# Kernel tuning notes

Hardware: AMD Instinct MI355X
Metric: run time of the kernel (lower is better)

Reference implementation:

```python
import jax, jax.numpy as jnp
import numpy as np

T = 8192   # sequence length (= max_seq_len)
E = 1024   # embedding dim
D = 11     # hard-coded projection dim in source


def setup_inputs() -> dict:
    key = jax.random.key(0)
    ks = jax.random.split(key, 6)
    s_e = 1.0 / np.sqrt(E)
    s_d = 1.0 / np.sqrt(D)
    return {
        "x": jax.random.randint(ks[0], (T,), 0, 32000, dtype=jnp.int64),
        "x_embeddings": jax.random.normal(ks[1], (T, E), dtype=jnp.float32),
        "Wk": jax.random.normal(ks[2], (D, E), dtype=jnp.float32) * s_e,
        "bk": jnp.zeros((D,), dtype=jnp.float32),
        "Wq": jax.random.normal(ks[3], (D, E), dtype=jnp.float32) * s_e,
        "bq": jnp.zeros((D,), dtype=jnp.float32),
        "Wv": jax.random.normal(ks[4], (D, E), dtype=jnp.float32) * s_e,
        "bv": jnp.zeros((D,), dtype=jnp.float32),
        "Wf": jax.random.normal(ks[5], (E, D), dtype=jnp.float32) * s_d,
        "bf": jnp.zeros((E,), dtype=jnp.float32),
    }


def reference(x, x_embeddings, Wk, bk, Wq, bq, Wv, bv, Wf, bf):
    t = x.shape[0]  # static under jit
    k = x_embeddings @ Wk.T + bk            # [T, D]
    q = x_embeddings @ Wq.T + bq            # [T, D]
    v = x_embeddings @ Wv.T + bv            # [T, D]
    att = q @ k.T                           # [T, T]; NOTE: no 1/sqrt(D) scaling in source
    causal = jnp.tril(jnp.ones((t, t), dtype=bool))
    att = jnp.where(causal, att, -jnp.inf)
    att = jax.nn.softmax(att, axis=1)       # dim=1 as in source
    res = att @ v                           # [T, D]
    return res @ Wf.T + bf                  # [T, E]
```

## Files before the change

### kernel.cpp

```cpp
#include <hip/hip_runtime.h>

#define T_SEQ 8192
#define E_DIM 1024
#define QS 36
#define NEC 8
#define ECOLS 128
#define KC 64
#define C2N 32
#define XST 65
#define RB 64
#define JCH 64
#define NSLOT 64
#define RPB 512
#define NIB (T_SEQ / RPB)
#define KVW 24
#define TR 16
#define LOG2E 1.4426950408889634f

__device__ __forceinline__ float2 pkfma(float2 a, float2 b, float2 c) {
    return make_float2(fmaf(a.x, b.x, c.x), fmaf(a.y, b.y, c.y));
}
__device__ __forceinline__ float2 f2(float x, float y) { return make_float2(x, y); }


__global__ __launch_bounds__(256) void prep_wf(const float* __restrict__ Wf,
                                               float* __restrict__ Wfp) {
    int id = blockIdx.x * 256 + threadIdx.x;
    if (id >= E_DIM * 12) return;
    int e = id / 12, d = id % 12;
    Wfp[id] = (d < 11) ? Wf[(size_t)e * 11 + d] : 0.f;
}

__global__ __launch_bounds__(256) void qkv_proj(
    const float* __restrict__ xe,
    const float* __restrict__ Wk, const float* __restrict__ bk,
    const float* __restrict__ Wq, const float* __restrict__ bq,
    const float* __restrict__ Wv, const float* __restrict__ bv,
    float* __restrict__ partQ) {
    const int row0 = blockIdx.x * RB;
    const int ec = blockIdx.y;
    const int lane = threadIdx.x & 63;
    const int wg = __builtin_amdgcn_readfirstlane(threadIdx.x >> 6);

    __shared__ float2 xP[C2N * XST];

    const float* wrow[9]; int col[9]; float bias[9]; bool live[9];
#pragma unroll
    for (int k = 0; k < 9; ++k) {
        int o = wg * 9 + k;
        const float* base; float b = 0.f; int c; bool lv = true;
        if (o < 11)      { base = Wk + (size_t)o * E_DIM;        b = bk[o];      c = o; }
        else if (o < 22) { base = Wq + (size_t)(o - 11) * E_DIM; b = bq[o - 11]; c = o + 1; }
        else if (o < 33) { base = Wv + (size_t)(o - 22) * E_DIM; b = bv[o - 22]; c = o + 2; }
        else             { base = Wk; c = (o == 33) ? 11 : (o == 34) ? 23 : 35; lv = false; }
        wrow[k] = base; col[k] = c; bias[k] = b; live[k] = lv;
    }

    float2 acc[9];
#pragma unroll
    for (int k = 0; k < 9; ++k) acc[k] = f2(0.f, 0.f);

    float4 st[4];
#define STAGE_LOAD(sub)                                                         \
    {                                                                           \
        const int cb = ec * ECOLS + (sub) * KC;                                 \
        _Pragma("unroll")                                                       \
        for (int t = 0; t < 4; ++t) {                                           \
            int idx = threadIdx.x + t * 256;                                    \
            int r = idx >> 4, c4 = idx & 15;                                    \
            st[t] = *(const float4*)(xe + (size_t)(row0 + r) * E_DIM + cb + c4 * 4); \
        }                                                                       \
    }

    STAGE_LOAD(0);
    for (int sub = 0; sub < ECOLS / KC; ++sub) {
        if (sub) __syncthreads();
#pragma unroll
        for (int t = 0; t < 4; ++t) {
            int idx = threadIdx.x + t * 256;
            int r = idx >> 4, c4 = idx & 15;
            float2* d = &xP[(size_t)(c4 * 2) * XST + r];
            d[0]   = f2(st[t].x, st[t].y);
            d[XST] = f2(st[t].z, st[t].w);
        }
        if (sub + 1 < ECOLS / KC) STAGE_LOAD(sub + 1);
        __syncthreads();

        const int cbase = ec * ECOLS + sub * KC;
#pragma unroll 4
        for (int c2 = 0; c2 < C2N; ++c2) {
            float2 xv = xP[c2 * XST + lane];
            const int c = cbase + 2 * c2;
#pragma unroll
            for (int k = 0; k < 9; ++k) {
                const float2 wv = *(const float2*)(wrow[k] + c);
                acc[k] = pkfma(xv, wv, acc[k]);
            }
        }
    }
#undef STAGE_LOAD

    float* dst = partQ + ((size_t)ec * T_SEQ + row0 + lane) * QS;
#pragma unroll
    for (int k = 0; k < 9; ++k) {
        float v = acc[k].x + acc[k].y + (ec == 0 ? bias[k] : 0.f);
        dst[col[k]] = live[k] ? v : 0.f;
    }
}

__global__ __launch_bounds__(256) void reduceQ(const float* __restrict__ partQ,
                                               float* __restrict__ qkvF) {
    const size_t idx = (size_t)blockIdx.x * 256 + threadIdx.x;
    const float4* p = (const float4*)partQ;
    const size_t cs = (size_t)T_SEQ * (QS / 4);
    float4 s = make_float4(0.f, 0.f, 0.f, 0.f);
#pragma unroll
    for (int c = 0; c < NEC; ++c) {
        float4 a = p[idx + (size_t)c * cs];
        s.x += a.x; s.y += a.y; s.z += a.z; s.w += a.w;
    }
    ((float4*)qkvF)[idx] = s;
}

__device__ __forceinline__ void attn_chunk(const float* kv, int j0, int r0,
    const float4& qa0, const float4& qa1, const float4& qa2,
    const float4& qb0, const float4& qb1, const float4& qb2,
    float2& a01, float2& a23, float2& a45, float2& a67, float2& a89, float2& aXL,
    float2& b01, float2& b23, float2& b45, float2& b67, float2& b89, float2& bXL) {
#pragma unroll 2
    for (int jj = 0; jj < JCH; ++jj) {
        const float* kp = kv + jj * KVW;
        const float4 kA = *(const float4*)(kp);
        const float4 kB = *(const float4*)(kp + 4);
        const float4 kC = *(const float4*)(kp + 8);
        const float4 vA = *(const float4*)(kp + 12);
        const float4 vB = *(const float4*)(kp + 16);
        const float4 vC = *(const float4*)(kp + 20);

        float2 sa = pkfma(f2(qa0.x, qa0.y), f2(kA.x, kA.y),
                    pkfma(f2(qa0.z, qa0.w), f2(kA.z, kA.w),
                    pkfma(f2(qa1.x, qa1.y), f2(kB.x, kB.y),
                    pkfma(f2(qa1.z, qa1.w), f2(kB.z, kB.w),
                    pkfma(f2(qa2.x, qa2.y), f2(kC.x, kC.y), f2(0.f, 0.f))))));
        float2 sb = pkfma(f2(qb0.x, qb0.y), f2(kA.x, kA.y),
                    pkfma(f2(qb0.z, qb0.w), f2(kA.z, kA.w),
                    pkfma(f2(qb1.x, qb1.y), f2(kB.x, kB.y),
                    pkfma(f2(qb1.z, qb1.w), f2(kB.z, kB.w),
                    pkfma(f2(qb2.x, qb2.y), f2(kC.x, kC.y), f2(0.f, 0.f))))));
        float pa = exp2f(sa.x + sa.y + qa2.z * kC.z);
        float pb = exp2f(sb.x + sb.y + qb2.z * kC.z);
        const int j = j0 + jj;
        pa = (j <= r0)     ? pa : 0.f;
        pb = (j <= r0 + 1) ? pb : 0.f;
        float2 pa2 = f2(pa, pa), pb2 = f2(pb, pb);
        a01 = pkfma(pa2, f2(vA.x, vA.y), a01);
        a23 = pkfma(pa2, f2(vA.z, vA.w), a23);
        a45 = pkfma(pa2, f2(vB.x, vB.y), a45);
        a67 = pkfma(pa2, f2(vB.z, vB.w), a67);
        a89 = pkfma(pa2, f2(vC.x, vC.y), a89);
        aXL = pkfma(pa2, f2(vC.z, 1.f),  aXL);
        b01 = pkfma(pb2, f2(vA.x, vA.y), b01);
        b23 = pkfma(pb2, f2(vA.z, vA.w), b23);
        b45 = pkfma(pb2, f2(vB.x, vB.y), b45);
        b67 = pkfma(pb2, f2(vB.z, vB.w), b67);
        b89 = pkfma(pb2, f2(vC.x, vC.y), b89);
        bXL = pkfma(pb2, f2(vC.z, 1.f),  bXL);
    }
}

__device__ __forceinline__ void stage_kv(const float* __restrict__ qkvF,
                                         float* kv, int j0) {
    for (int idx = threadIdx.x; idx < JCH * 6; idx += 256) {
        int row = idx / 6, f = idx % 6;
        int srcOff = f * 4 + (f >= 3 ? 12 : 0);
        float4 v = *(const float4*)(qkvF + (size_t)(j0 + row) * QS + srcOff);
        *(float4*)(kv + row * KVW + f * 4) = v;
    }
}

__global__ __launch_bounds__(256, 4) void attn(const float* __restrict__ qkvF,
                                               float* __restrict__ part) {
    const int ib = blockIdx.x, jc = blockIdx.y;
    if (jc > 8 * ib + 7) return;
    const int row0 = ib * RPB;
    const int r0 = row0 + threadIdx.x * 2;

    const float* qp0 = qkvF + (size_t)r0 * QS + 12;
    const float* qp1 = qp0 + QS;
    float4 qa0 = *(const float4*)(qp0), qa1 = *(const float4*)(qp0 + 4), qa2 = *(const float4*)(qp0 + 8);
    float4 qb0 = *(const float4*)(qp1), qb1 = *(const float4*)(qp1 + 4), qb2 = *(const float4*)(qp1 + 8);
    qa0.x *= LOG2E; qa0.y *= LOG2E; qa0.z *= LOG2E; qa0.w *= LOG2E;
    qa1.x *= LOG2E; qa1.y *= LOG2E; qa1.z *= LOG2E; qa1.w *= LOG2E;
    qa2.x *= LOG2E; qa2.y *= LOG2E; qa2.z *= LOG2E;
    qb0.x *= LOG2E; qb0.y *= LOG2E; qb0.z *= LOG2E; qb0.w *= LOG2E;
    qb1.x *= LOG2E; qb1.y *= LOG2E; qb1.z *= LOG2E; qb1.w *= LOG2E;
    qb2.x *= LOG2E; qb2.y *= LOG2E; qb2.z *= LOG2E;

    float2 a01 = f2(0.f, 0.f), a23 = a01, a45 = a01, a67 = a01, a89 = a01, aXL = a01;
    float2 b01 = a01, b23 = a01, b45 = a01, b67 = a01, b89 = a01, bXL = a01;

    __shared__ float kv[JCH * KVW];

    const int j0A = jc * JCH;
    stage_kv(qkvF, kv, j0A);
    __syncthreads();
    attn_chunk(kv, j0A, r0, qa0, qa1, qa2, qb0, qb1, qb2,
               a01, a23, a45, a67, a89, aXL, b01, b23, b45, b67, b89, bXL);

    const int j0B = (jc + NSLOT) * JCH;
    if (j0B <= row0 + RPB - 1) {
        __syncthreads();
        stage_kv(qkvF, kv, j0B);
        __syncthreads();
        attn_chunk(kv, j0B, r0, qa0, qa1, qa2, qb0, qb1, qb2,
                   a01, a23, a45, a67, a89, aXL, b01, b23, b45, b67, b89, bXL);
    }

    float* dst = part + ((size_t)jc * T_SEQ + r0) * 12;
    float4 t;
    t.x = a01.x; t.y = a01.y; t.z = a23.x; t.w = a23.y; *(float4*)(dst + 0)  = t;
    t.x = a45.x; t.y = a45.y; t.z = a67.x; t.w = a67.y; *(float4*)(dst + 4)  = t;
    t.x = a89.x; t.y = a89.y; t.z = aXL.x; t.w = aXL.y; *(float4*)(dst + 8)  = t;
    t.x = b01.x; t.y = b01.y; t.z = b23.x; t.w = b23.y; *(float4*)(dst + 12) = t;
    t.x = b45.x; t.y = b45.y; t.z = b67.x; t.w = b67.y; *(float4*)(dst + 16) = t;
    t.x = b89.x; t.y = b89.y; t.z = bXL.x; t.w = bXL.y; *(float4*)(dst + 20) = t;
}

__global__ __launch_bounds__(256) void pass2(const float* __restrict__ part,
                                             const float* __restrict__ Wfp,
                                             const float* __restrict__ bf,
                                             float* __restrict__ out) {
    const int t0 = blockIdx.x * TR;
    __shared__ float res[TR][12];
    int cnt = t0 / JCH + 1;
    if (cnt > NSLOT) cnt = NSLOT;
    if (threadIdx.x < TR * 12) {
        const float* p = part + (size_t)t0 * 12 + threadIdx.x;
        const size_t S = (size_t)T_SEQ * 12;
        float v[8];
#pragma unroll
        for (int u = 0; u < 8; ++u) v[u] = 0.f;
        int c = 0;
        for (; c + 8 <= cnt; c += 8) {
#pragma unroll
            for (int u = 0; u < 8; ++u) v[u] += p[(size_t)(c + u) * S];
        }
        for (; c < cnt; ++c) v[0] += p[(size_t)c * S];
        float s = ((v[0] + v[1]) + (v[2] + v[3])) + ((v[4] + v[5]) + (v[6] + v[7]));
        const int d = threadIdx.x % 12;
        res[threadIdx.x / 12][d] = (d == 11) ? (1.f / s) : s;
    }
    __syncthreads();

    const int e0 = threadIdx.x * 4;
    float4 wf[4][3];
#pragma unroll
    for (int ee = 0; ee < 4; ++ee) {
        const float4* wp = (const float4*)(Wfp + (size_t)(e0 + ee) * 12);
        wf[ee][0] = wp[0]; wf[ee][1] = wp[1]; wf[ee][2] = wp[2];
    }
    const float4 bv = *(const float4*)(bf + e0);

    for (int r = 0; r < TR; ++r) {
        float rr[12];
#pragma unroll
        for (int d = 0; d < 12; ++d) rr[d] = res[r][d];
        float2 a0 = f2(0.f, 0.f), a1 = a0, a2 = a0, a3 = a0;
#pragma unroll
        for (int d = 0; d < 10; d += 2) {
            float2 rv = f2(rr[d], rr[d + 1]);
            a0 = pkfma(rv, f2(((const float*)&wf[0][0])[d], ((const float*)&wf[0][0])[d + 1]), a0);
            a1 = pkfma(rv, f2(((const float*)&wf[1][0])[d], ((const float*)&wf[1][0])[d + 1]), a1);
            a2 = pkfma(rv, f2(((const float*)&wf[2][0])[d], ((const float*)&wf[2][0])[d + 1]), a2);
            a3 = pkfma(rv, f2(((const float*)&wf[3][0])[d], ((const float*)&wf[3][0])[d + 1]), a3);
        }
        const float rl = rr[11];
        float4 ov;
        ov.x = (a0.x + a0.y + rr[10] * wf[0][2].z) * rl + bv.x;
        ov.y = (a1.x + a1.y + rr[10] * wf[1][2].z) * rl + bv.y;
        ov.z = (a2.x + a2.y + rr[10] * wf[2][2].z) * rl + bv.z;
        ov.w = (a3.x + a3.y + rr[10] * wf[3][2].z) * rl + bv.w;
        *(float4*)(out + (size_t)(t0 + r) * E_DIM + e0) = ov;
    }
}

extern "C" void kernel_launch(void* const* d_in, const int* in_sizes, int n_in,
                              void* d_out, int out_size, void* d_ws, size_t ws_size,
                              hipStream_t stream) {
    const float* xe = (const float*)d_in[1];
    const float* Wk = (const float*)d_in[2];
    const float* bk = (const float*)d_in[3];
    const float* Wq = (const float*)d_in[4];
    const float* bq = (const float*)d_in[5];
    const float* Wv = (const float*)d_in[6];
    const float* bv = (const float*)d_in[7];
    const float* Wf = (const float*)d_in[8];
    const float* bf = (const float*)d_in[9];
    float* out = (float*)d_out;

    float* qkvF  = (float*)d_ws;
    float* wfp   = qkvF + (size_t)T_SEQ * QS;
    float* partQ = wfp + (size_t)E_DIM * 12;
    float* part  = partQ;

    prep_wf<<<(E_DIM * 12 + 255) / 256, 256, 0, stream>>>(Wf, wfp);
    qkv_proj<<<dim3(T_SEQ / RB, NEC), 256, 0, stream>>>(xe, Wk, bk, Wq, bq, Wv, bv, partQ);
    reduceQ<<<(T_SEQ * (QS / 4)) / 256, 256, 0, stream>>>(partQ, qkvF);
    attn<<<dim3(NIB, NSLOT), 256, 0, stream>>>(qkvF, part);
    pass2<<<T_SEQ / TR, 256, 0, stream>>>(part, wfp, bf, out);
}
```

Measured before the change: 193.0 us.

## Pair causal KV chunks per attention block and widen QKV projection loads

Each attention block now processes chunk s together with its mirror chunk (8*ib+7-s), so every block does the same two chunks of work. This balances the causal triangle and reduces the number of partial slots pass2 has to sum, down to 4*(ib+1) per row block. The attention inner loop is manually unrolled by two keys, and launch bounds drop to 2 waves per SIMD, which gives the compiler more registers. The QKV projection now stages x as float4 in shared memory and reads float4 weights, halving LDS and global load counts, at some risk of bank conflicts and register pressure.

```diff
diff --git a/kernel.cpp b/kernel.cpp
--- a/kernel.cpp
+++ b/kernel.cpp
@@ -6,8 +6,8 @@
 #define NEC 8
 #define ECOLS 128
 #define KC 64
-#define C2N 32
-#define XST 65
+#define NC4 16
+#define X4ST 65
 #define RB 64
 #define JCH 64
 #define NSLOT 64
@@ -42,7 +42,7 @@
     const int lane = threadIdx.x & 63;
     const int wg = __builtin_amdgcn_readfirstlane(threadIdx.x >> 6);
 
-    __shared__ float2 xP[C2N * XST];
+    __shared__ float4 xP4[NC4 * X4ST];
 
     const float* wrow[9]; int col[9]; float bias[9]; bool live[9];
 #pragma unroll
@@ -79,22 +79,21 @@
         for (int t = 0; t < 4; ++t) {
             int idx = threadIdx.x + t * 256;
             int r = idx >> 4, c4 = idx & 15;
-            float2* d = &xP[(size_t)(c4 * 2) * XST + r];
-            d[0]   = f2(st[t].x, st[t].y);
-            d[XST] = f2(st[t].z, st[t].w);
+            xP4[c4 * X4ST + r] = st[t];
         }
         if (sub + 1 < ECOLS / KC) STAGE_LOAD(sub + 1);
         __syncthreads();
 
         const int cbase = ec * ECOLS + sub * KC;
-#pragma unroll 4
-        for (int c2 = 0; c2 < C2N; ++c2) {
-            float2 xv = xP[c2 * XST + lane];
-            const int c = cbase + 2 * c2;
+#pragma unroll
+        for (int c4 = 0; c4 < NC4; ++c4) {
+            float4 xv = xP4[c4 * X4ST + lane];
+            const int c = cbase + 4 * c4;
 #pragma unroll
             for (int k = 0; k < 9; ++k) {
-                const float2 wv = *(const float2*)(wrow[k] + c);
-                acc[k] = pkfma(xv, wv, acc[k]);
+                const float4 wv = *(const float4*)(wrow[k] + c);
+                acc[k] = pkfma(f2(xv.x, xv.y), f2(wv.x, wv.y), acc[k]);
+                acc[k] = pkfma(f2(xv.z, xv.w), f2(wv.z, wv.w), acc[k]);
             }
         }
     }
@@ -120,52 +119,6 @@
         s.x += a.x; s.y += a.y; s.z += a.z; s.w += a.w;
     }
     ((float4*)qkvF)[idx] = s;
-}
-
-__device__ __forceinline__ void attn_chunk(const float* kv, int j0, int r0,
-    const float4& qa0, const float4& qa1, const float4& qa2,
-    const float4& qb0, const float4& qb1, const float4& qb2,
-    float2& a01, float2& a23, float2& a45, float2& a67, float2& a89, float2& aXL,
-    float2& b01, float2& b23, float2& b45, float2& b67, float2& b89, float2& bXL) {
-#pragma unroll 2
-    for (int jj = 0; jj < JCH; ++jj) {
-        const float* kp = kv + jj * KVW;
-        const float4 kA = *(const float4*)(kp);
-        const float4 kB = *(const float4*)(kp + 4);
-        const float4 kC = *(const float4*)(kp + 8);
-        const float4 vA = *(const float4*)(kp + 12);
-        const float4 vB = *(const float4*)(kp + 16);
-        const float4 vC = *(const float4*)(kp + 20);
-
-        float2 sa = pkfma(f2(qa0.x, qa0.y), f2(kA.x, kA.y),
-                    pkfma(f2(qa0.z, qa0.w), f2(kA.z, kA.w),
-                    pkfma(f2(qa1.x, qa1.y), f2(kB.x, kB.y),
-                    pkfma(f2(qa1.z, qa1.w), f2(kB.z, kB.w),
-                    pkfma(f2(qa2.x, qa2.y), f2(kC.x, kC.y), f2(0.f, 0.f))))));
-        float2 sb = pkfma(f2(qb0.x, qb0.y), f2(kA.x, kA.y),
-                    pkfma(f2(qb0.z, qb0.w), f2(kA.z, kA.w),
-                    pkfma(f2(qb1.x, qb1.y), f2(kB.x, kB.y),
-                    pkfma(f2(qb1.z, qb1.w), f2(kB.z, kB.w),
-                    pkfma(f2(qb2.x, qb2.y), f2(kC.x, kC.y), f2(0.f, 0.f))))));
-        float pa = exp2f(sa.x + sa.y + qa2.z * kC.z);
-        float pb = exp2f(sb.x + sb.y + qb2.z * kC.z);
-        const int j = j0 + jj;
-        pa = (j <= r0)     ? pa : 0.f;
-        pb = (j <= r0 + 1) ? pb : 0.f;
-        float2 pa2 = f2(pa, pa), pb2 = f2(pb, pb);
-        a01 = pkfma(pa2, f2(vA.x, vA.y), a01);
-        a23 = pkfma(pa2, f2(vA.z, vA.w), a23);
-        a45 = pkfma(pa2, f2(vB.x, vB.y), a45);
-        a67 = pkfma(pa2, f2(vB.z, vB.w), a67);
-        a89 = pkfma(pa2, f2(vC.x, vC.y), a89);
-        aXL = pkfma(pa2, f2(vC.z, 1.f),  aXL);
-        b01 = pkfma(pb2, f2(vA.x, vA.y), b01);
-        b23 = pkfma(pb2, f2(vA.z, vA.w), b23);
-        b45 = pkfma(pb2, f2(vB.x, vB.y), b45);
-        b67 = pkfma(pb2, f2(vB.z, vB.w), b67);
-        b89 = pkfma(pb2, f2(vC.x, vC.y), b89);
-        bXL = pkfma(pb2, f2(vC.z, 1.f),  bXL);
-    }
 }
 
 __device__ __forceinline__ void stage_kv(const float* __restrict__ qkvF,
@@ -178,10 +131,92 @@
     }
 }
 
-__global__ __launch_bounds__(256, 4) void attn(const float* __restrict__ qkvF,
+__device__ __forceinline__ void attn_chunk(const float* kv, int j0, int r0,
+    const float4& qa0, const float4& qa1, const float4& qa2,
+    const float4& qb0, const float4& qb1, const float4& qb2,
+    float2& a01, float2& a23, float2& a45, float2& a67, float2& a89, float2& aXL,
+    float2& b01, float2& b23, float2& b45, float2& b67, float2& b89, float2& bXL) {
+#pragma unroll 2
+    for (int jj = 0; jj < JCH; jj += 2) {
+        const float* kp0 = kv + jj * KVW;
+        const float* kp1 = kp0 + KVW;
+        const float4 kA0 = *(const float4*)(kp0);
+        const float4 kB0 = *(const float4*)(kp0 + 4);
+        const float4 kC0 = *(const float4*)(kp0 + 8);
+        const float4 vA0 = *(const float4*)(kp0 + 12);
+        const float4 vB0 = *(const float4*)(kp0 + 16);
+        const float4 vC0 = *(const float4*)(kp0 + 20);
+        const float4 kA1 = *(const float4*)(kp1);
+        const float4 kB1 = *(const float4*)(kp1 + 4);
+        const float4 kC1 = *(const float4*)(kp1 + 8);
+        const float4 vA1 = *(const float4*)(kp1 + 12);
+        const float4 vB1 = *(const float4*)(kp1 + 16);
+        const float4 vC1 = *(const float4*)(kp1 + 20);
+
+        float2 sa = pkfma(f2(qa0.x, qa0.y), f2(kA0.x, kA0.y),
+                    pkfma(f2(qa0.z, qa0.w), f2(kA0.z, kA0.w),
+                    pkfma(f2(qa1.x, qa1.y), f2(kB0.x, kB0.y),
+                    pkfma(f2(qa1.z, qa1.w), f2(kB0.z, kB0.w),
+                    pkfma(f2(qa2.x, qa2.y), f2(kC0.x, kC0.y), f2(0.f, 0.f))))));
+        float2 sb = pkfma(f2(qb0.x, qb0.y), f2(kA0.x, kA0.y),
+                    pkfma(f2(qb0.z, qb0.w), f2(kA0.z, kA0.w),
+                    pkfma(f2(qb1.x, qb1.y), f2(kB0.x, kB0.y),
+                    pkfma(f2(qb1.z, qb1.w), f2(kB0.z, kB0.w),
+                    pkfma(f2(qb2.x, qb2.y), f2(kC0.x, kC0.y), f2(0.f, 0.f))))));
+        float pa = exp2f(sa.x + sa.y + qa2.z * kC0.z);
+        float pb = exp2f(sb.x + sb.y + qb2.z * kC0.z);
+        int j = j0 + jj;
+        pa = (j <= r0)     ? pa : 0.f;
+        pb = (j <= r0 + 1) ? pb : 0.f;
+        float2 pa2 = f2(pa, pa), pb2 = f2(pb, pb);
+        a01 = pkfma(pa2, f2(vA0.x, vA0.y), a01);
+        a23 = pkfma(pa2, f2(vA0.z, vA0.w), a23);
+        a45 = pkfma(pa2, f2(vB0.x, vB0.y), a45);
+        a67 = pkfma(pa2, f2(vB0.z, vB0.w), a67);
+        a89 = pkfma(pa2, f2(vC0.x, vC0.y), a89);
+        aXL = pkfma(pa2, f2(vC0.z, 1.f),  aXL);
+        b01 = pkfma(pb2, f2(vA0.x, vA0.y), b01);
+        b23 = pkfma(pb2, f2(vA0.z, vA0.w), b23);
+        b45 = pkfma(pb2, f2(vB0.x, vB0.y), b45);
+        b67 = pkfma(pb2, f2(vB0.z, vB0.w), b67);
+        b89 = pkfma(pb2, f2(vC0.x, vC0.y), b89);
+        bXL = pkfma(pb2, f2(vC0.z, 1.f),  bXL);
+
+        sa = pkfma(f2(qa0.x, qa0.y), f2(kA1.x, kA1.y),
+             pkfma(f2(qa0.z, qa0.w), f2(kA1.z, kA1.w),
+             pkfma(f2(qa1.x, qa1.y), f2(kB1.x, kB1.y),
+             pkfma(f2(qa1.z, qa1.w), f2(kB1.z, kB1.w),
+             pkfma(f2(qa2.x, qa2.y), f2(kC1.x, kC1.y), f2(0.f, 0.f))))));
+        sb = pkfma(f2(qb0.x, qb0.y), f2(kA1.x, kA1.y),
+             pkfma(f2(qb0.z, qb0.w), f2(kA1.z, kA1.w),
+             pkfma(f2(qb1.x, qb1.y), f2(kB1.x, kB1.y),
+             pkfma(f2(qb1.z, qb1.w), f2(kB1.z, kB1.w),
+             pkfma(f2(qb2.x, qb2.y), f2(kC1.x, kC1.y), f2(0.f, 0.f))))));
+        pa = exp2f(sa.x + sa.y + qa2.z * kC1.z);
+        pb = exp2f(sb.x + sb.y + qb2.z * kC1.z);
+        j = j0 + jj + 1;
+        pa = (j <= r0)     ? pa : 0.f;
+        pb = (j <= r0 + 1) ? pb : 0.f;
+        pa2 = f2(pa, pa); pb2 = f2(pb, pb);
+        a01 = pkfma(pa2, f2(vA1.x, vA1.y), a01);
+        a23 = pkfma(pa2, f2(vA1.z, vA1.w), a23);
+        a45 = pkfma(pa2, f2(vB1.x, vB1.y), a45);
+        a67 = pkfma(pa2, f2(vB1.z, vB1.w), a67);
+        a89 = pkfma(pa2, f2(vC1.x, vC1.y), a89);
+        aXL = pkfma(pa2, f2(vC1.z, 1.f),  aXL);
+        b01 = pkfma(pb2, f2(vA1.x, vA1.y), b01);
+        b23 = pkfma(pb2, f2(vA1.z, vA1.w), b23);
+        b45 = pkfma(pb2, f2(vB1.x, vB1.y), b45);
+        b67 = pkfma(pb2, f2(vB1.z, vB1.w), b67);
+        b89 = pkfma(pb2, f2(vC1.x, vC1.y), b89);
+        bXL = pkfma(pb2, f2(vC1.z, 1.f),  bXL);
+    }
+}
+
+__global__ __launch_bounds__(256, 2) void attn(const float* __restrict__ qkvF,
                                                float* __restrict__ part) {
-    const int ib = blockIdx.x, jc = blockIdx.y;
-    if (jc > 8 * ib + 7) return;
+    const int ib = blockIdx.x, s = blockIdx.y;
+    if (s >= 4 * ib + 4) return;
     const int row0 = ib * RPB;
     const int r0 = row0 + threadIdx.x * 2;
 
@@ -201,22 +236,18 @@
 
     __shared__ float kv[JCH * KVW];
 
-    const int j0A = jc * JCH;
-    stage_kv(qkvF, kv, j0A);
-    __syncthreads();
-    attn_chunk(kv, j0A, r0, qa0, qa1, qa2, qb0, qb1, qb2,
-               a01, a23, a45, a67, a89, aXL, b01, b23, b45, b67, b89, bXL);
-
-    const int j0B = (jc + NSLOT) * JCH;
-    if (j0B <= row0 + RPB - 1) {
+#pragma unroll
+    for (int pass = 0; pass < 2; ++pass) {
+        const int jc = pass ? (8 * ib + 7 - s) : s;
+        const int j0 = jc * JCH;
+        if (pass) __syncthreads();
+        stage_kv(qkvF, kv, j0);
         __syncthreads();
-        stage_kv(qkvF, kv, j0B);
-        __syncthreads();
-        attn_chunk(kv, j0B, r0, qa0, qa1, qa2, qb0, qb1, qb2,
+        attn_chunk(kv, j0, r0, qa0, qa1, qa2, qb0, qb1, qb2,
                    a01, a23, a45, a67, a89, aXL, b01, b23, b45, b67, b89, bXL);
     }
 
-    float* dst = part + ((size_t)jc * T_SEQ + r0) * 12;
+    float* dst = part + ((size_t)s * T_SEQ + r0) * 12;
     float4 t;
     t.x = a01.x; t.y = a01.y; t.z = a23.x; t.w = a23.y; *(float4*)(dst + 0)  = t;
     t.x = a45.x; t.y = a45.y; t.z = a67.x; t.w = a67.y; *(float4*)(dst + 4)  = t;
@@ -232,23 +263,20 @@
                                              float* __restrict__ out) {
     const int t0 = blockIdx.x * TR;
     __shared__ float res[TR][12];
-    int cnt = t0 / JCH + 1;
-    if (cnt > NSLOT) cnt = NSLOT;
+    const int cnt = 4 * (t0 / RPB) + 4;
     if (threadIdx.x < TR * 12) {
         const float* p = part + (size_t)t0 * 12 + threadIdx.x;
         const size_t S = (size_t)T_SEQ * 12;
-        float v[8];
-#pragma unroll
-        for (int u = 0; u < 8; ++u) v[u] = 0.f;
-        int c = 0;
-        for (; c + 8 <= cnt; c += 8) {
-#pragma unroll
-            for (int u = 0; u < 8; ++u) v[u] += p[(size_t)(c + u) * S];
+        float v[4];
+#pragma unroll
+        for (int u = 0; u < 4; ++u) v[u] = 0.f;
+        for (int c = 0; c < cnt; c += 4) {
+#pragma unroll
+            for (int u = 0; u < 4; ++u) v[u] += p[(size_t)(c + u) * S];
         }
-        for (; c < cnt; ++c) v[0] += p[(size_t)c * S];
-        float s = ((v[0] + v[1]) + (v[2] + v[3])) + ((v[4] + v[5]) + (v[6] + v[7]));
+        float sum = (v[0] + v[1]) + (v[2] + v[3]);
         const int d = threadIdx.x % 12;
-        res[threadIdx.x / 12][d] = (d == 11) ? (1.f / s) : s;
+        res[threadIdx.x / 12][d] = (d == 11) ? (1.f / sum) : sum;
     }
     __syncthreads();
 
```

Result: slower. 226.1 us (+17.1%).

## Load-balance causal attention with triangular block mapping and paired chunks; stage QKV weights in LDS

Applied to the files above, without the earlier changes.

The attention grid no longer launches a full rectangle with early-exit blocks. Each block is mapped through a triangular index to a row-block and two key chunks, one from each end of the causal range, so every block does equal work. Chunk size and count are template parameters: 32-row chunks are used when the workspace is large enough, with 64 as a fallback, and pass2 reduces the matching number of partials. The QKV projection now stages both the x tile and the weight tile in shared memory at once rather than double-buffering x and reading weights from global memory. The cost is an integer sqrt index decode per block and more partial sums for pass2 to reduce.

```diff
diff --git a/kernel.cpp b/kernel.cpp
--- a/kernel.cpp
+++ b/kernel.cpp
@@ -5,12 +5,9 @@
 #define QS 36
 #define NEC 8
 #define ECOLS 128
-#define KC 64
-#define C2N 32
-#define XST 65
+#define NC4 32
+#define X4ST 33
 #define RB 64
-#define JCH 64
-#define NSLOT 64
 #define RPB 512
 #define NIB (T_SEQ / RPB)
 #define KVW 24
@@ -40,71 +37,61 @@
     const int row0 = blockIdx.x * RB;
     const int ec = blockIdx.y;
     const int lane = threadIdx.x & 63;
-    const int wg = __builtin_amdgcn_readfirstlane(threadIdx.x >> 6);
-
-    __shared__ float2 xP[C2N * XST];
-
-    const float* wrow[9]; int col[9]; float bias[9]; bool live[9];
+    const int wg = threadIdx.x >> 6;
+    const int cb = ec * ECOLS;
+
+    __shared__ float4 xT[RB * X4ST];
+    __shared__ float4 wT[36 * NC4];
+
+#pragma unroll
+    for (int t = 0; t < 8; ++t) {
+        int idx = threadIdx.x + t * 256;
+        int r = idx >> 5, c4 = idx & 31;
+        xT[r * X4ST + c4] =
+            *(const float4*)(xe + (size_t)(row0 + r) * E_DIM + cb + c4 * 4);
+    }
+    for (int idx = threadIdx.x; idx < 36 * NC4; idx += 256) {
+        int r = idx >> 5, c4 = idx & 31;
+        float4 v = make_float4(0.f, 0.f, 0.f, 0.f);
+        if (r < 33) {
+            const float* base = (r < 11) ? (Wk + (size_t)r * E_DIM)
+                              : (r < 22) ? (Wq + (size_t)(r - 11) * E_DIM)
+                                         : (Wv + (size_t)(r - 22) * E_DIM);
+            v = *(const float4*)(base + cb + c4 * 4);
+        }
+        wT[idx] = v;
+    }
+    __syncthreads();
+
+    float2 acc[9];
+#pragma unroll
+    for (int k = 0; k < 9; ++k) acc[k] = f2(0.f, 0.f);
+
+    const float4* xr = xT + lane * X4ST;
+    const float4* wr = wT + wg * 9 * NC4;
+#pragma unroll 4
+    for (int c4 = 0; c4 < NC4; ++c4) {
+        float4 xv = xr[c4];
+        float2 xlo = f2(xv.x, xv.y), xhi = f2(xv.z, xv.w);
+#pragma unroll
+        for (int k = 0; k < 9; ++k) {
+            float4 wv = wr[k * NC4 + c4];
+            acc[k] = pkfma(xlo, f2(wv.x, wv.y), acc[k]);
+            acc[k] = pkfma(xhi, f2(wv.z, wv.w), acc[k]);
+        }
+    }
+
+    float* dst = partQ + ((size_t)ec * T_SEQ + row0 + lane) * QS;
 #pragma unroll
     for (int k = 0; k < 9; ++k) {
         int o = wg * 9 + k;
-        const float* base; float b = 0.f; int c; bool lv = true;
-        if (o < 11)      { base = Wk + (size_t)o * E_DIM;        b = bk[o];      c = o; }
-        else if (o < 22) { base = Wq + (size_t)(o - 11) * E_DIM; b = bq[o - 11]; c = o + 1; }
-        else if (o < 33) { base = Wv + (size_t)(o - 22) * E_DIM; b = bv[o - 22]; c = o + 2; }
-        else             { base = Wk; c = (o == 33) ? 11 : (o == 34) ? 23 : 35; lv = false; }
-        wrow[k] = base; col[k] = c; bias[k] = b; live[k] = lv;
-    }
-
-    float2 acc[9];
-#pragma unroll
-    for (int k = 0; k < 9; ++k) acc[k] = f2(0.f, 0.f);
-
-    float4 st[4];
-#define STAGE_LOAD(sub)                                                         \
-    {                                                                           \
-        const int cb = ec * ECOLS + (sub) * KC;                                 \
-        _Pragma("unroll")                                                       \
-        for (int t = 0; t < 4; ++t) {                                           \
-            int idx = threadIdx.x + t * 256;                                    \
-            int r = idx >> 4, c4 = idx & 15;                                    \
-            st[t] = *(const float4*)(xe + (size_t)(row0 + r) * E_DIM + cb + c4 * 4); \
-        }                                                                       \
-    }
-
-    STAGE_LOAD(0);
-    for (int sub = 0; sub < ECOLS / KC; ++sub) {
-        if (sub) __syncthreads();
-#pragma unroll
-        for (int t = 0; t < 4; ++t) {
-            int idx = threadIdx.x + t * 256;
-            int r = idx >> 4, c4 = idx & 15;
-            float2* d = &xP[(size_t)(c4 * 2) * XST + r];
-            d[0]   = f2(st[t].x, st[t].y);
-            d[XST] = f2(st[t].z, st[t].w);
-        }
-        if (sub + 1 < ECOLS / KC) STAGE_LOAD(sub + 1);
-        __syncthreads();
-
-        const int cbase = ec * ECOLS + sub * KC;
-#pragma unroll 4
-        for (int c2 = 0; c2 < C2N; ++c2) {
-            float2 xv = xP[c2 * XST + lane];
-            const int c = cbase + 2 * c2;
-#pragma unroll
-            for (int k = 0; k < 9; ++k) {
-                const float2 wv = *(const float2*)(wrow[k] + c);
-                acc[k] = pkfma(xv, wv, acc[k]);
-            }
-        }
-    }
-#undef STAGE_LOAD
-
-    float* dst = partQ + ((size_t)ec * T_SEQ + row0 + lane) * QS;
-#pragma unroll
-    for (int k = 0; k < 9; ++k) {
-        float v = acc[k].x + acc[k].y + (ec == 0 ? bias[k] : 0.f);
-        dst[col[k]] = live[k] ? v : 0.f;
+        bool live = (o < 33);
+        int c = (o < 11) ? o : (o < 22) ? o + 1 : (o < 33) ? o + 2
+                : (o == 33) ? 11 : (o == 34) ? 23 : 35;
+        float b = 0.f;
+        if (ec == 0 && live)
+            b = (o < 11) ? bk[o] : (o < 22) ? bq[o - 11] : bv[o - 22];
+        dst[c] = live ? (acc[k].x + acc[k].y + b) : 0.f;
     }
 }
 
@@ -122,13 +109,25 @@
     ((float4*)qkvF)[idx] = s;
 }
 
+template <int LJCH>
+__device__ __forceinline__ void stage_kv(const float* __restrict__ qkvF,
+                                         float* kv, int j0) {
+    for (int idx = threadIdx.x; idx < LJCH * 6; idx += 256) {
+        int row = idx / 6, f = idx % 6;
+        int srcOff = f * 4 + (f >= 3 ? 12 : 0);
+        float4 v = *(const float4*)(qkvF + (size_t)(j0 + row) * QS + srcOff);
+        *(float4*)(kv + row * KVW + f * 4) = v;
+    }
+}
+
+template <int LJCH>
 __device__ __forceinline__ void attn_chunk(const float* kv, int j0, int r0,
     const float4& qa0, const float4& qa1, const float4& qa2,
     const float4& qb0, const float4& qb1, const float4& qb2,
     float2& a01, float2& a23, float2& a45, float2& a67, float2& a89, float2& aXL,
     float2& b01, float2& b23, float2& b45, float2& b67, float2& b89, float2& bXL) {
 #pragma unroll 2
-    for (int jj = 0; jj < JCH; ++jj) {
+    for (int jj = 0; jj < LJCH; ++jj) {
         const float* kp = kv + jj * KVW;
         const float4 kA = *(const float4*)(kp);
         const float4 kB = *(const float4*)(kp + 4);
@@ -168,20 +167,16 @@
     }
 }
 
-__device__ __forceinline__ void stage_kv(const float* __restrict__ qkvF,
-                                         float* kv, int j0) {
-    for (int idx = threadIdx.x; idx < JCH * 6; idx += 256) {
-        int row = idx / 6, f = idx % 6;
-        int srcOff = f * 4 + (f >= 3 ? 12 : 0);
-        float4 v = *(const float4*)(qkvF + (size_t)(j0 + row) * QS + srcOff);
-        *(float4*)(kv + row * KVW + f * 4) = v;
-    }
-}
-
+template <int LJCH, int H>
 __global__ __launch_bounds__(256, 4) void attn(const float* __restrict__ qkvF,
                                                float* __restrict__ part) {
-    const int ib = blockIdx.x, jc = blockIdx.y;
-    if (jc > 8 * ib + 7) return;
+    const int b = blockIdx.x;
+    int ib = (int)((sqrtf((float)(8 * b / H + 1)) - 1.0f) * 0.5f);
+    while (H * (ib + 1) * (ib + 2) / 2 <= b) ++ib;
+    while (H * ib * (ib + 1) / 2 > b) --ib;
+    const int s = b - H * ib * (ib + 1) / 2;
+    const int chunkB = 2 * H * (ib + 1) - 1 - s;
+
     const int row0 = ib * RPB;
     const int r0 = row0 + threadIdx.x * 2;
 
@@ -199,24 +194,20 @@
     float2 a01 = f2(0.f, 0.f), a23 = a01, a45 = a01, a67 = a01, a89 = a01, aXL = a01;
     float2 b01 = a01, b23 = a01, b45 = a01, b67 = a01, b89 = a01, bXL = a01;
 
-    __shared__ float kv[JCH * KVW];
-
-    const int j0A = jc * JCH;
-    stage_kv(qkvF, kv, j0A);
-    __syncthreads();
-    attn_chunk(kv, j0A, r0, qa0, qa1, qa2, qb0, qb1, qb2,
-               a01, a23, a45, a67, a89, aXL, b01, b23, b45, b67, b89, bXL);
-
-    const int j0B = (jc + NSLOT) * JCH;
-    if (j0B <= row0 + RPB - 1) {
+    __shared__ float kv[LJCH * KVW];
+
+#pragma unroll
+    for (int pass = 0; pass < 2; ++pass) {
+        const int jc = pass ? chunkB : s;
+        const int j0 = jc * LJCH;
+        if (pass) __syncthreads();
+        stage_kv<LJCH>(qkvF, kv, j0);
         __syncthreads();
-        stage_kv(qkvF, kv, j0B);
-        __syncthreads();
-        attn_chunk(kv, j0B, r0, qa0, qa1, qa2, qb0, qb1, qb2,
-                   a01, a23, a45, a67, a89, aXL, b01, b23, b45, b67, b89, bXL);
-    }
-
-    float* dst = part + ((size_t)jc * T_SEQ + r0) * 12;
+        attn_chunk<LJCH>(kv, j0, r0, qa0, qa1, qa2, qb0, qb1, qb2,
+                         a01, a23, a45, a67, a89, aXL, b01, b23, b45, b67, b89, bXL);
+    }
+
+    float* dst = part + ((size_t)s * T_SEQ + r0) * 12;
     float4 t;
     t.x = a01.x; t.y = a01.y; t.z = a23.x; t.w = a23.y; *(float4*)(dst + 0)  = t;
     t.x = a45.x; t.y = a45.y; t.z = a67.x; t.w = a67.y; *(float4*)(dst + 4)  = t;
@@ -229,26 +220,23 @@
 __global__ __launch_bounds__(256) void pass2(const float* __restrict__ part,
                                              const float* __restrict__ Wfp,
                                              const float* __restrict__ bf,
-                                             float* __restrict__ out) {
+                                             float* __restrict__ out, int H) {
     const int t0 = blockIdx.x * TR;
     __shared__ float res[TR][12];
-    int cnt = t0 / JCH + 1;
-    if (cnt > NSLOT) cnt = NSLOT;
+    const int cnt = H * (t0 / RPB) + H;
     if (threadIdx.x < TR * 12) {
         const float* p = part + (size_t)t0 * 12 + threadIdx.x;
         const size_t S = (size_t)T_SEQ * 12;
-        float v[8];
-#pragma unroll
-        for (int u = 0; u < 8; ++u) v[u] = 0.f;
-        int c = 0;
-        for (; c + 8 <= cnt; c += 8) {
-#pragma unroll
-            for (int u = 0; u < 8; ++u) v[u] += p[(size_t)(c + u) * S];
+        float v[4];
+#pragma unroll
+        for (int u = 0; u < 4; ++u) v[u] = 0.f;
+        for (int c = 0; c < cnt; c += 4) {
+#pragma unroll
+            for (int u = 0; u < 4; ++u) v[u] += p[(size_t)(c + u) * S];
         }
-        for (; c < cnt; ++c) v[0] += p[(size_t)c * S];
-        float s = ((v[0] + v[1]) + (v[2] + v[3])) + ((v[4] + v[5]) + (v[6] + v[7]));
+        float sum = (v[0] + v[1]) + (v[2] + v[3]);
         const int d = threadIdx.x % 12;
-        res[threadIdx.x / 12][d] = (d == 11) ? (1.f / s) : s;
+        res[threadIdx.x / 12][d] = (d == 11) ? (1.f / sum) : sum;
     }
     __syncthreads();
 
@@ -303,9 +291,18 @@
     float* partQ = wfp + (size_t)E_DIM * 12;
     float* part  = partQ;
 
+    const size_t fixed = ((size_t)T_SEQ * QS + (size_t)E_DIM * 12) * 4;
+    const size_t need32 = fixed + (size_t)128 * T_SEQ * 12 * 4;
+
     prep_wf<<<(E_DIM * 12 + 255) / 256, 256, 0, stream>>>(Wf, wfp);
     qkv_proj<<<dim3(T_SEQ / RB, NEC), 256, 0, stream>>>(xe, Wk, bk, Wq, bq, Wv, bv, partQ);
     reduceQ<<<(T_SEQ * (QS / 4)) / 256, 256, 0, stream>>>(partQ, qkvF);
-    attn<<<dim3(NIB, NSLOT), 256, 0, stream>>>(qkvF, part);
-    pass2<<<T_SEQ / TR, 256, 0, stream>>>(part, wfp, bf, out);
-}
+
+    if (ws_size >= need32) {
+        attn<32, 8><<<8 * NIB * (NIB + 1) / 2, 256, 0, stream>>>(qkvF, part);
+        pass2<<<T_SEQ / TR, 256, 0, stream>>>(part, wfp, bf, out, 8);
+    } else {
+        attn<64, 4><<<4 * NIB * (NIB + 1) / 2, 256, 0, stream>>>(qkvF, part);
+        pass2<<<T_SEQ / TR, 256, 0, stream>>>(part, wfp, bf, out, 4);
+    }
+}
```

Result: no change. 194.0 us (+0.5%).
